# Performance work log

Measured on AMD Instinct MI355X. Metric: run time of the kernel, lower is better.

Reference implementation:

```python
import jax, jax.numpy as jnp
import numpy as np

B, S, D = 2, 2048, 1024  # batch, seq, model_dim
E, K, H = 8, 2, 4096     # experts, top_k, expert hidden
CAP_FACTOR = 1.0


def setup_inputs() -> dict:
    key = jax.random.key(0)
    ks = jax.random.split(key, 6)
    scale_in = 1.0 / np.sqrt(D)
    scale_h = 1.0 / np.sqrt(H)
    return {
        "x": jax.random.normal(ks[0], (B, S, D), jnp.float32),
        "wg": jax.random.normal(ks[1], (D, E), jnp.float32) * scale_in,
        "w1": jax.random.normal(ks[2], (E, D, H), jnp.float32) * scale_in,
        "b1": jnp.zeros((E, H), jnp.float32),
        "w2": jax.random.normal(ks[3], (E, H, D), jnp.float32) * scale_h,
        "b2": jnp.zeros((E, D), jnp.float32),
    }


def _moe_forward(x, wg, w1, b1, w2, b2):
    Bb, Ss, Dd = x.shape
    T = Bb * Ss
    cap = int(K * CAP_FACTOR * ((T + E - 1) // E))  # Tutel capacity rule
    xt = x.reshape(T, Dd)

    # ---- gating ----
    logits = xt @ wg                      # [T, E]
    scores = jax.nn.softmax(logits, axis=-1)
    gates_k, idx_k = jax.lax.top_k(scores, K)  # [T, K]
    # normalize_gate=True: renormalize top-k gates
    gates_k = gates_k / jnp.sum(gates_k, axis=-1, keepdims=True)

    # ---- GShard-style location assignment (slot-major cumsum) ----
    masks = jax.nn.one_hot(idx_k, E, dtype=jnp.int32)           # [T, K, E]
    m = jnp.transpose(masks, (1, 0, 2)).reshape(K * T, E)       # slot-major
    locs_full = jnp.cumsum(m, axis=0) - 1                       # [K*T, E]
    loc = jnp.sum(locs_full * m, axis=-1)                       # [K*T]
    loc = loc.reshape(K, T).T                                   # [T, K]
    valid = (loc < cap).astype(xt.dtype)                        # capacity drop
    loc_c = jnp.clip(loc, 0, cap - 1)

    # ---- dispatch: scatter tokens into [E, cap, D] ----
    contrib = (xt[:, None, :] * valid[:, :, None]).reshape(T * K, Dd)
    disp = jnp.zeros((E, cap, Dd), xt.dtype)
    disp = disp.at[idx_k.reshape(-1), loc_c.reshape(-1)].add(contrib)

    # ---- grouped expert FFN ----
    h = jax.nn.relu(jnp.einsum("ecd,edh->ech", disp, w1) + b1[:, None, :])
    out = jnp.einsum("ech,ehd->ecd", h, w2) + b2[:, None, :]

    # ---- combine (postscore): gather + gate-weighted sum ----
    gathered = out[idx_k, loc_c]                                # [T, K, D]
    y = jnp.einsum("tk,tkd->td", gates_k * valid, gathered)
    return y.reshape(Bb, Ss, Dd)


def reference(x, wg, w1, b1, w2, b2):
    return _moe_forward(x, wg, w1, b1, w2, b2)
```

## Files before the change

kernel.cpp:

```cpp
#include <hip/hip_runtime.h>
#include <stdint.h>

#define NTOK 4096
#define DIM  1024
#define NEXP 8
#define HID  4096
#define CAP  1024

typedef __bf16 bf16x8 __attribute__((ext_vector_type(8)));
typedef float  f32x4  __attribute__((ext_vector_type(4)));

__device__ __forceinline__ unsigned short f2bf(float f) {
  unsigned int u = __float_as_uint(f);
  return (unsigned short)((u + 0x7fffu + ((u >> 16) & 1u)) >> 16);
}

__device__ __forceinline__ float bf2f(unsigned int bits16) {
  return __uint_as_float(bits16 << 16);
}

__device__ __forceinline__ void load_lds16(const void* g, void* l) {
  __builtin_amdgcn_global_load_lds(
      (__attribute__((address_space(1))) void*)g,
      (__attribute__((address_space(3))) void*)l,
      16, 0, 0);
}

__global__ void gating_kernel(const float* __restrict__ x, const float* __restrict__ wg,
                              int* __restrict__ tok_e, float* __restrict__ tok_g) {
  const int t = blockIdx.x;
  const int l = threadIdx.x;
  float acc[NEXP];
#pragma unroll
  for (int e = 0; e < NEXP; ++e) acc[e] = 0.f;

  const float4* x4  = (const float4*)(x + (size_t)t * DIM);
  const float4* wg4 = (const float4*)wg;
#pragma unroll
  for (int i = 0; i < 4; ++i) {
    int dq = i * 64 + l;
    float4 xv = x4[dq];
    float xs[4] = {xv.x, xv.y, xv.z, xv.w};
#pragma unroll
    for (int c = 0; c < 4; ++c) {
      int d = dq * 4 + c;
      float4 wa = wg4[d * 2], wb = wg4[d * 2 + 1];
      acc[0] += xs[c] * wa.x; acc[1] += xs[c] * wa.y;
      acc[2] += xs[c] * wa.z; acc[3] += xs[c] * wa.w;
      acc[4] += xs[c] * wb.x; acc[5] += xs[c] * wb.y;
      acc[6] += xs[c] * wb.z; acc[7] += xs[c] * wb.w;
    }
  }
#pragma unroll
  for (int off = 32; off; off >>= 1)
#pragma unroll
    for (int e = 0; e < NEXP; ++e) acc[e] += __shfl_xor(acc[e], off);

  if (l == 0) {
    float m = acc[0];
#pragma unroll
    for (int e = 1; e < NEXP; ++e) m = fmaxf(m, acc[e]);
    float p[NEXP];
#pragma unroll
    for (int e = 0; e < NEXP; ++e) p[e] = __expf(acc[e] - m);
    int e0 = 0; float b0 = p[0];
#pragma unroll
    for (int e = 1; e < NEXP; ++e) if (p[e] > b0) { b0 = p[e]; e0 = e; }
    int e1 = -1; float b1v = -1.f;
#pragma unroll
    for (int e = 0; e < NEXP; ++e) if (e != e0 && p[e] > b1v) { b1v = p[e]; e1 = e; }
    float inv = 1.f / (b0 + b1v);
    tok_e[2 * t] = e0; tok_e[2 * t + 1] = e1;
    tok_g[2 * t] = b0 * inv; tok_g[2 * t + 1] = b1v * inv;
  }
}

__global__ void scan_kernel(const int* __restrict__ tok_e, int* __restrict__ tok_loc,
                            int* __restrict__ slot_map) {
  const int l = threadIdx.x;
  const unsigned long long below = (1ull << l) - 1ull;
  int base[NEXP];
#pragma unroll
  for (int e = 0; e < NEXP; ++e) base[e] = 0;

  int nxt = tok_e[((0 * 64 + l) & (NTOK - 1)) * 2 + ((0 * 64 + l) >> 12)];
  for (int it = 0; it < 128; ++it) {
    int e = nxt;
    if (it + 1 < 128) {
      int g2 = (it + 1) * 64 + l;
      nxt = tok_e[(g2 & (NTOK - 1)) * 2 + (g2 >> 12)];
    }
    int loc = 0;
#pragma unroll
    for (int ex = 0; ex < NEXP; ++ex) {
      unsigned long long msk = __ballot(e == ex);
      int off = __popcll(msk & below);
      if (e == ex) loc = base[ex] + off;
      base[ex] += __popcll(msk);
    }
    int g = it * 64 + l;
    int k = g >> 12, t = g & (NTOK - 1);
    bool valid = loc < CAP;
    tok_loc[t * 2 + k] = valid ? loc : -1;
    if (valid) slot_map[e * CAP + loc] = t;
  }
#pragma unroll
  for (int ex = 0; ex < NEXP; ++ex) {
    int c = base[ex] < CAP ? base[ex] : CAP;
    for (int i = c + l; i < CAP; i += 64) slot_map[ex * CAP + i] = -1;
  }
}

__global__ void dispatch_kernel(const float* __restrict__ x, const int* __restrict__ slot_map,
                                unsigned short* __restrict__ disp) {
  const int s = blockIdx.x;
  const int tid = threadIdx.x;
  int t = slot_map[s];
  uint2 o;
  if (t >= 0) {
    float4 v = ((const float4*)(x + (size_t)t * DIM))[tid];
    o.x = (unsigned)f2bf(v.x) | ((unsigned)f2bf(v.y) << 16);
    o.y = (unsigned)f2bf(v.z) | ((unsigned)f2bf(v.w) << 16);
  } else {
    o.x = 0u; o.y = 0u;
  }
  ((uint2*)(disp + (size_t)s * DIM))[tid] = o;
}

__global__ void transpose_cvt(const float* __restrict__ in, unsigned short* __restrict__ out,
                              int R, int C) {
  __shared__ float tile[64][65];
  const int e = blockIdx.z;
  const float* inp = in + (size_t)e * R * C;
  unsigned short* outp = out + (size_t)e * R * C;
  const int c0 = blockIdx.x * 64, r0 = blockIdx.y * 64;
  const int t = threadIdx.x;
#pragma unroll
  for (int i = 0; i < 4; ++i) {
    int idx = i * 256 + t;
    int r = idx >> 4, c4 = (idx & 15) * 4;
    float4 v = *(const float4*)(inp + (size_t)(r0 + r) * C + c0 + c4);
    tile[r][c4 + 0] = v.x; tile[r][c4 + 1] = v.y;
    tile[r][c4 + 2] = v.z; tile[r][c4 + 3] = v.w;
  }
  __syncthreads();
#pragma unroll
  for (int i = 0; i < 2; ++i) {
    int idx = i * 256 + t;
    int c = idx >> 3, r8 = (idx & 7) * 8;
    unsigned short s[8];
#pragma unroll
    for (int j = 0; j < 8; ++j) s[j] = f2bf(tile[r8 + j][c]);
    uint4 o;
    o.x = (unsigned)s[0] | ((unsigned)s[1] << 16);
    o.y = (unsigned)s[2] | ((unsigned)s[3] << 16);
    o.z = (unsigned)s[4] | ((unsigned)s[5] << 16);
    o.w = (unsigned)s[6] | ((unsigned)s[7] << 16);
    *(uint4*)(outp + (size_t)(c0 + c) * R + r0 + r8) = o;
  }
}

template <bool RELU, int MB, int NB>
__global__ __launch_bounds__(256)
void gemm_kernel(const unsigned short* __restrict__ A, const unsigned short* __restrict__ B,
                 const float* __restrict__ bias, unsigned short* __restrict__ C,
                 int N, int K) {
  constexpr int M = 1024;
  const int bid = blockIdx.x;
  const int e = bid / (MB * NB);
  const int r = bid - e * (MB * NB);
  const int patch = r / (MB * 4);
  const int q = r - patch * (MB * 4);
  const int mtile = q >> 2;
  const int ntile = patch * 4 + (q & 3);

  A += (size_t)e * M * K;
  B += (size_t)e * N * K;
  bias += (size_t)e * N;
  C += (size_t)e * M * N;
  const int m0 = mtile * 128;
  const int n0 = ntile * 128;
  const int tid = threadIdx.x;
  const int wave = tid >> 6, lane = tid & 63;
  const int wm = wave >> 1, wn = wave & 1;

  __shared__ __align__(16) unsigned short As[2][128 * 64];
  __shared__ __align__(16) unsigned short Bs[2][128 * 64];

  const int srow = lane >> 3;
  const int scol = ((lane & 7) ^ (srow & 7)) * 8;
  const unsigned short* gA = A + (size_t)(m0 + wave * 8 + srow) * K + scol;
  const unsigned short* gB = B + (size_t)(n0 + wave * 8 + srow) * K + scol;
  const int lbase = (wave * 8) * 64;

  f32x4 acc[4][4] = {};

  const int quad = lane >> 4;
  const int lxor = lane & 7;
  const int arowb = (wm * 64 + (lane & 15)) * 64;
  const int browb = (wn * 64 + (lane & 15)) * 64;

#pragma unroll
  for (int i = 0; i < 4; ++i) {
    load_lds16(gA + (size_t)i * 32 * K, &As[0][lbase + i * 32 * 64]);
    load_lds16(gB + (size_t)i * 32 * K, &Bs[0][lbase + i * 32 * 64]);
  }
  gA += 64; gB += 64;

  const int nIter = K >> 6;
  for (int it = 0; it < nIter; ++it) {
    const int cur = it & 1;
    __syncthreads();
    if (it + 1 < nIter) {
#pragma unroll
      for (int i = 0; i < 4; ++i) {
        load_lds16(gA + (size_t)i * 32 * K, &As[cur ^ 1][lbase + i * 32 * 64]);
        load_lds16(gB + (size_t)i * 32 * K, &Bs[cur ^ 1][lbase + i * 32 * 64]);
      }
      gA += 64; gB += 64;
    }
#pragma unroll
    for (int kk = 0; kk < 64; kk += 32) {
      const int coff = ((quad + (kk >> 3)) ^ lxor) * 8;
      bf16x8 af[4], bfr[4];
#pragma unroll
      for (int i = 0; i < 4; ++i)
        af[i] = *reinterpret_cast<const bf16x8*>(&As[cur][arowb + i * 16 * 64 + coff]);
#pragma unroll
      for (int j = 0; j < 4; ++j)
        bfr[j] = *reinterpret_cast<const bf16x8*>(&Bs[cur][browb + j * 16 * 64 + coff]);
#pragma unroll
      for (int i = 0; i < 4; ++i)
#pragma unroll
        for (int j = 0; j < 4; ++j)
          acc[i][j] = __builtin_amdgcn_mfma_f32_16x16x32_bf16(af[i], bfr[j], acc[i][j], 0, 0, 0);
    }
  }

  __syncthreads();
  unsigned short* scr = (wave < 2 ? &As[0][0] : &Bs[0][0]) + (wave & 1) * 4608;
  const int lc = lane & 15;
#pragma unroll
  for (int j = 0; j < 4; ++j) {
    float bj = bias[n0 + wn * 64 + j * 16 + lc];
#pragma unroll
    for (int i = 0; i < 4; ++i)
#pragma unroll
      for (int rr = 0; rr < 4; ++rr) {
        float v = acc[i][j][rr] + bj;
        if (RELU) v = fmaxf(v, 0.f);
        scr[(i * 16 + quad * 4 + rr) * 72 + j * 16 + lc] = f2bf(v);
      }
  }
  __asm__ volatile("s_waitcnt lgkmcnt(0)" ::: "memory");
  const int erow = lane >> 3;
  const int ecol = (lane & 7) * 8;
  unsigned short* Cbase = C + (size_t)(m0 + wm * 64) * N + n0 + wn * 64;
#pragma unroll
  for (int p = 0; p < 8; ++p) {
    uint4 v = *(const uint4*)&scr[(p * 8 + erow) * 72 + ecol];
    *(uint4*)&Cbase[(size_t)(p * 8 + erow) * N + ecol] = v;
  }
}

__global__ void combine_kernel(const unsigned short* __restrict__ outb,
                               const int* __restrict__ tok_e, const int* __restrict__ tok_loc,
                               const float* __restrict__ tok_g, float* __restrict__ y) {
  const int t = blockIdx.x;
  const int tid = threadIdx.x;
  int e0 = tok_e[2 * t], e1 = tok_e[2 * t + 1];
  int l0 = tok_loc[2 * t], l1 = tok_loc[2 * t + 1];
  float g0 = tok_g[2 * t], g1 = tok_g[2 * t + 1];
  float ax = 0.f, ay = 0.f, az = 0.f, aw = 0.f;
  if (l0 >= 0) {
    uint2 u = ((const uint2*)(outb + ((size_t)e0 * CAP + l0) * DIM))[tid];
    ax += g0 * bf2f(u.x & 0xffffu); ay += g0 * __uint_as_float(u.x & 0xffff0000u);
    az += g0 * bf2f(u.y & 0xffffu); aw += g0 * __uint_as_float(u.y & 0xffff0000u);
  }
  if (l1 >= 0) {
    uint2 u = ((const uint2*)(outb + ((size_t)e1 * CAP + l1) * DIM))[tid];
    ax += g1 * bf2f(u.x & 0xffffu); ay += g1 * __uint_as_float(u.x & 0xffff0000u);
    az += g1 * bf2f(u.y & 0xffffu); aw += g1 * __uint_as_float(u.y & 0xffff0000u);
  }
  float4 o; o.x = ax; o.y = ay; o.z = az; o.w = aw;
  ((float4*)(y + (size_t)t * DIM))[tid] = o;
}

extern "C" void kernel_launch(void* const* d_in, const int* in_sizes, int n_in,
                              void* d_out, int out_size, void* d_ws, size_t ws_size,
                              hipStream_t stream) {
  const float* x  = (const float*)d_in[0];
  const float* wg = (const float*)d_in[1];
  const float* w1 = (const float*)d_in[2];
  const float* b1 = (const float*)d_in[3];
  const float* w2 = (const float*)d_in[4];
  const float* b2 = (const float*)d_in[5];
  float* y = (float*)d_out;

  char* ws = (char*)d_ws;
  int*   tok_e    = (int*)(ws);
  int*   tok_loc  = (int*)(ws + 32768);
  float* tok_g    = (float*)(ws + 65536);
  int*   slot_map = (int*)(ws + 98304);
  unsigned short* disp = (unsigned short*)(ws + 131072);
  unsigned short* wbuf = (unsigned short*)(ws + 131072 + (16ull << 20));
  unsigned short* h    = (unsigned short*)(ws + 131072 + (80ull << 20));
  unsigned short* outb = (unsigned short*)(ws + 131072 + (144ull << 20));

  gating_kernel<<<NTOK, 64, 0, stream>>>(x, wg, tok_e, tok_g);
  scan_kernel<<<1, 64, 0, stream>>>(tok_e, tok_loc, slot_map);
  dispatch_kernel<<<NEXP * CAP, 256, 0, stream>>>(x, slot_map, disp);
  transpose_cvt<<<dim3(HID / 64, DIM / 64, NEXP), 256, 0, stream>>>(w1, wbuf, DIM, HID);
  gemm_kernel<true, 8, 32><<<NEXP * 8 * 32, 256, 0, stream>>>(disp, wbuf, b1, h, HID, DIM);
  transpose_cvt<<<dim3(DIM / 64, HID / 64, NEXP), 256, 0, stream>>>(w2, wbuf, HID, DIM);
  gemm_kernel<false, 8, 8><<<NEXP * 8 * 8, 256, 0, stream>>>(h, wbuf, b2, outb, DIM, HID);
  combine_kernel<<<NTOK, 256, 0, stream>>>(outb, tok_e, tok_loc, tok_g, y);
}
```

Before: 541.4 us.

## Rewrite expert GEMMs as 8-wave large-tile kernels with 4-phase pipelined LDS staging

Replaces the 128x128 4-wave expert GEMM with a 512-thread kernel using 256x256 tiles for the first GEMM and 128x256 for the second. The K loop is split into four quadrant phases, each issuing the next global-to-LDS loads while running MFMAs, with explicit vmcnt waits, barriers and setprio. The goal is more data reuse per tile and overlap of memory traffic with tensor-core work. The cost is large dynamic shared memory (up to 128KB), hence low occupancy and fewer blocks for the second GEMM (256 blocks), plus fragile hand-written wait counts.

```diff
diff --git a/kernel.cpp b/kernel.cpp
--- a/kernel.cpp
+++ b/kernel.cpp
@@ -160,106 +160,160 @@
   }
 }
 
-template <bool RELU, int MB, int NB>
-__global__ __launch_bounds__(256)
-void gemm_kernel(const unsigned short* __restrict__ A, const unsigned short* __restrict__ B,
-                 const float* __restrict__ bias, unsigned short* __restrict__ C,
-                 int N, int K) {
+template <int BM, int BN, bool RELU>
+__global__ __launch_bounds__(512)
+void gemm8(const unsigned short* __restrict__ A, const unsigned short* __restrict__ B,
+           const float* __restrict__ bias, unsigned short* __restrict__ C,
+           int N, int K) {
   constexpr int M = 1024;
+  constexpr int FR = BM / 64;
+  constexpr int FC = BN / 128;
+  constexpr int ASLOT = (BM / 2) * 64;
+  constexpr int BSLOT = (BN / 2) * 64;
+  constexpr int LA = BM / 128;
+  constexpr int LB = BN / 128;
+  static_assert(LA + LB == 4 || LA + LB == 3, "vmcnt literal");
+
+  extern __shared__ __align__(16) unsigned short smem[];
+  unsigned short* As = smem;
+  unsigned short* Bs = smem + 4 * ASLOT;
+
+  const int mt = M / BM;
+  const int ntn = N / BN;
   const int bid = blockIdx.x;
-  const int e = bid / (MB * NB);
-  const int r = bid - e * (MB * NB);
-  const int patch = r / (MB * 4);
-  const int q = r - patch * (MB * 4);
-  const int mtile = q >> 2;
-  const int ntile = patch * 4 + (q & 3);
+  const int e = bid / (mt * ntn);
+  const int rb = bid - e * mt * ntn;
+  const int mtile = rb / ntn;
+  const int ntile = rb - mtile * ntn;
 
   A += (size_t)e * M * K;
   B += (size_t)e * N * K;
   bias += (size_t)e * N;
   C += (size_t)e * M * N;
-  const int m0 = mtile * 128;
-  const int n0 = ntile * 128;
+  const int m0 = mtile * BM;
+  const int n0 = ntile * BN;
+
   const int tid = threadIdx.x;
-  const int wave = tid >> 6, lane = tid & 63;
-  const int wm = wave >> 1, wn = wave & 1;
-
-  __shared__ __align__(16) unsigned short As[2][128 * 64];
-  __shared__ __align__(16) unsigned short Bs[2][128 * 64];
+  const int w = tid >> 6, lane = tid & 63;
+  const int wm = w >> 2, wn = w & 3;
 
   const int srow = lane >> 3;
-  const int scol = ((lane & 7) ^ (srow & 7)) * 8;
-  const unsigned short* gA = A + (size_t)(m0 + wave * 8 + srow) * K + scol;
-  const unsigned short* gB = B + (size_t)(n0 + wave * 8 + srow) * K + scol;
-  const int lbase = (wave * 8) * 64;
-
-  f32x4 acc[4][4] = {};
-
-  const int quad = lane >> 4;
-  const int lxor = lane & 7;
-  const int arowb = (wm * 64 + (lane & 15)) * 64;
-  const int browb = (wn * 64 + (lane & 15)) * 64;
-
-#pragma unroll
-  for (int i = 0; i < 4; ++i) {
-    load_lds16(gA + (size_t)i * 32 * K, &As[0][lbase + i * 32 * 64]);
-    load_lds16(gB + (size_t)i * 32 * K, &Bs[0][lbase + i * 32 * 64]);
-  }
-  gA += 64; gB += 64;
-
-  const int nIter = K >> 6;
-  for (int it = 0; it < nIter; ++it) {
-    const int cur = it & 1;
+  const int scol = ((lane & 7) ^ srow) * 8;
+  const unsigned short* gA = A + (size_t)(m0 + w * 8 + srow) * K + scol;
+  const unsigned short* gB = B + (size_t)(n0 + w * 8 + srow) * K + scol;
+  const int lbase = w * 512;
+
+  const int arow0 = wm * (BM / 4) + (lane & 15);
+  const int brow0 = wn * (BN / 8) + (lane & 15);
+  const int c0 = (((lane >> 4) + 0) ^ (lane & 7)) * 8;
+  const int c1 = (((lane >> 4) + 4) ^ (lane & 7)) * 8;
+
+  f32x4 acc[2][2][FR][FC] = {};
+  const int nt = K >> 6;
+
+#define STAGE_A(T, MH) do {                                                        \
+    const unsigned short* g_ = gA + (size_t)((MH) * (BM / 2)) * K + (size_t)(T) * 64; \
+    unsigned short* l_ = &As[(2 * ((T) & 1) + (MH)) * ASLOT + lbase];              \
+    _Pragma("unroll")                                                              \
+    for (int q_ = 0; q_ < LA; ++q_)                                                \
+      load_lds16(g_ + (size_t)q_ * 64 * K, l_ + q_ * 4096);                        \
+  } while (0)
+
+#define STAGE_B(T, NH) do {                                                        \
+    const unsigned short* g_ = gB + (size_t)((NH) * (BN / 2)) * K + (size_t)(T) * 64; \
+    unsigned short* l_ = &Bs[(2 * ((T) & 1) + (NH)) * BSLOT + lbase];              \
+    _Pragma("unroll")                                                              \
+    for (int q_ = 0; q_ < LB; ++q_)                                                \
+      load_lds16(g_ + (size_t)q_ * 64 * K, l_ + q_ * 4096);                        \
+  } while (0)
+
+#define WAIT_VMN() do {                                                            \
+    if constexpr (LA + LB == 4) asm volatile("s_waitcnt vmcnt(4)" ::: "memory");   \
+    else                        asm volatile("s_waitcnt vmcnt(3)" ::: "memory");   \
+  } while (0)
+
+#define PHASE(MH, NH, ISVM, ...) do {                                              \
+    bf16x8 af[FR][2], bfv[FC][2];                                                  \
+    const unsigned short* ab_ = &As[(2 * cur + (MH)) * ASLOT + arow0 * 64];        \
+    const unsigned short* bb_ = &Bs[(2 * cur + (NH)) * BSLOT + brow0 * 64];        \
+    _Pragma("unroll")                                                              \
+    for (int f_ = 0; f_ < FR; ++f_) {                                              \
+      af[f_][0] = *(const bf16x8*)(ab_ + f_ * 1024 + c0);                          \
+      af[f_][1] = *(const bf16x8*)(ab_ + f_ * 1024 + c1);                          \
+    }                                                                              \
+    _Pragma("unroll")                                                              \
+    for (int f_ = 0; f_ < FC; ++f_) {                                              \
+      bfv[f_][0] = *(const bf16x8*)(bb_ + f_ * 1024 + c0);                         \
+      bfv[f_][1] = *(const bf16x8*)(bb_ + f_ * 1024 + c1);                         \
+    }                                                                              \
+    __VA_ARGS__                                                                    \
+    __builtin_amdgcn_s_barrier();                                                  \
+    asm volatile("s_waitcnt lgkmcnt(0)" ::: "memory");                             \
+    __builtin_amdgcn_sched_barrier(0);                                             \
+    __builtin_amdgcn_s_setprio(1);                                                 \
+    _Pragma("unroll")                                                              \
+    for (int f_ = 0; f_ < FR; ++f_)                                                \
+      _Pragma("unroll")                                                            \
+      for (int g_ = 0; g_ < FC; ++g_) {                                            \
+        acc[MH][NH][f_][g_] = __builtin_amdgcn_mfma_f32_16x16x32_bf16(             \
+            af[f_][0], bfv[g_][0], acc[MH][NH][f_][g_], 0, 0, 0);                  \
+        acc[MH][NH][f_][g_] = __builtin_amdgcn_mfma_f32_16x16x32_bf16(             \
+            af[f_][1], bfv[g_][1], acc[MH][NH][f_][g_], 0, 0, 0);                  \
+      }                                                                            \
+    __builtin_amdgcn_s_setprio(0);                                                 \
+    if (ISVM) WAIT_VMN();                                                          \
+    asm volatile("" ::: "memory");                                                 \
+    __builtin_amdgcn_s_barrier();                                                  \
+  } while (0)
+
+  STAGE_A(0, 0); STAGE_A(0, 1); STAGE_B(0, 0); STAGE_B(0, 1);
+  STAGE_B(1, 0); STAGE_A(1, 0);
+  WAIT_VMN();
+  __builtin_amdgcn_s_barrier();
+
+  for (int t = 0; t < nt; ++t) {
+    const int cur = t & 1;
+    const bool s1 = (t + 1) < nt, s2 = (t + 2) < nt;
+    PHASE(0, 0, false, if (s1) STAGE_A(t + 1, 1); );
+    PHASE(1, 0, false, if (s1) STAGE_B(t + 1, 1); );
+    PHASE(0, 1, false, if (s2) STAGE_B(t + 2, 0); );
+    PHASE(1, 1, true,  if (s2) STAGE_A(t + 2, 0); );
+  }
+
+#undef PHASE
+#undef WAIT_VMN
+#undef STAGE_B
+#undef STAGE_A
+
+  const int lc = lane & 15, quad = lane >> 4;
+  constexpr int SW = BN + 8;
+  unsigned short* scr = smem;
+#pragma unroll
+  for (int Mh = 0; Mh < 2; ++Mh) {
     __syncthreads();
-    if (it + 1 < nIter) {
-#pragma unroll
-      for (int i = 0; i < 4; ++i) {
-        load_lds16(gA + (size_t)i * 32 * K, &As[cur ^ 1][lbase + i * 32 * 64]);
-        load_lds16(gB + (size_t)i * 32 * K, &Bs[cur ^ 1][lbase + i * 32 * 64]);
-      }
-      gA += 64; gB += 64;
+#pragma unroll
+    for (int Nh = 0; Nh < 2; ++Nh)
+#pragma unroll
+      for (int f = 0; f < FR; ++f)
+#pragma unroll
+        for (int g = 0; g < FC; ++g) {
+          float bv = bias[n0 + Nh * (BN / 2) + wn * (BN / 8) + g * 16 + lc];
+#pragma unroll
+          for (int r2 = 0; r2 < 4; ++r2) {
+            float v = acc[Mh][Nh][f][g][r2] + bv;
+            if (RELU) v = fmaxf(v, 0.f);
+            scr[(wm * (BM / 4) + f * 16 + quad * 4 + r2) * SW +
+                Nh * (BN / 2) + wn * (BN / 8) + g * 16 + lc] = f2bf(v);
+          }
+        }
+    __syncthreads();
+#pragma unroll
+    for (int it = 0; it < (BM / 2) * (BN / 8) / 512; ++it) {
+      const int u = it * 512 + tid;
+      const int row = u / (BN / 8), seg = u % (BN / 8);
+      uint4 v = *(const uint4*)&scr[row * SW + seg * 8];
+      *(uint4*)&C[(size_t)(m0 + Mh * (BM / 2) + row) * N + n0 + seg * 8] = v;
     }
-#pragma unroll
-    for (int kk = 0; kk < 64; kk += 32) {
-      const int coff = ((quad + (kk >> 3)) ^ lxor) * 8;
-      bf16x8 af[4], bfr[4];
-#pragma unroll
-      for (int i = 0; i < 4; ++i)
-        af[i] = *reinterpret_cast<const bf16x8*>(&As[cur][arowb + i * 16 * 64 + coff]);
-#pragma unroll
-      for (int j = 0; j < 4; ++j)
-        bfr[j] = *reinterpret_cast<const bf16x8*>(&Bs[cur][browb + j * 16 * 64 + coff]);
-#pragma unroll
-      for (int i = 0; i < 4; ++i)
-#pragma unroll
-        for (int j = 0; j < 4; ++j)
-          acc[i][j] = __builtin_amdgcn_mfma_f32_16x16x32_bf16(af[i], bfr[j], acc[i][j], 0, 0, 0);
-    }
-  }
-
-  __syncthreads();
-  unsigned short* scr = (wave < 2 ? &As[0][0] : &Bs[0][0]) + (wave & 1) * 4608;
-  const int lc = lane & 15;
-#pragma unroll
-  for (int j = 0; j < 4; ++j) {
-    float bj = bias[n0 + wn * 64 + j * 16 + lc];
-#pragma unroll
-    for (int i = 0; i < 4; ++i)
-#pragma unroll
-      for (int rr = 0; rr < 4; ++rr) {
-        float v = acc[i][j][rr] + bj;
-        if (RELU) v = fmaxf(v, 0.f);
-        scr[(i * 16 + quad * 4 + rr) * 72 + j * 16 + lc] = f2bf(v);
-      }
-  }
-  __asm__ volatile("s_waitcnt lgkmcnt(0)" ::: "memory");
-  const int erow = lane >> 3;
-  const int ecol = (lane & 7) * 8;
-  unsigned short* Cbase = C + (size_t)(m0 + wm * 64) * N + n0 + wn * 64;
-#pragma unroll
-  for (int p = 0; p < 8; ++p) {
-    uint4 v = *(const uint4*)&scr[(p * 8 + erow) * 72 + ecol];
-    *(uint4*)&Cbase[(size_t)(p * 8 + erow) * N + ecol] = v;
   }
 }
 
@@ -307,12 +361,23 @@
   unsigned short* h    = (unsigned short*)(ws + 131072 + (80ull << 20));
   unsigned short* outb = (unsigned short*)(ws + 131072 + (144ull << 20));
 
+  static int att = 0;
+  if (!att) {
+    (void)hipFuncSetAttribute(reinterpret_cast<const void*>(&gemm8<256, 256, true>),
+                              hipFuncAttributeMaxDynamicSharedMemorySize, 131072);
+    (void)hipFuncSetAttribute(reinterpret_cast<const void*>(&gemm8<128, 256, false>),
+                              hipFuncAttributeMaxDynamicSharedMemorySize, 98304);
+    att = 1;
+  }
+
   gating_kernel<<<NTOK, 64, 0, stream>>>(x, wg, tok_e, tok_g);
   scan_kernel<<<1, 64, 0, stream>>>(tok_e, tok_loc, slot_map);
   dispatch_kernel<<<NEXP * CAP, 256, 0, stream>>>(x, slot_map, disp);
   transpose_cvt<<<dim3(HID / 64, DIM / 64, NEXP), 256, 0, stream>>>(w1, wbuf, DIM, HID);
-  gemm_kernel<true, 8, 32><<<NEXP * 8 * 32, 256, 0, stream>>>(disp, wbuf, b1, h, HID, DIM);
+  gemm8<256, 256, true><<<NEXP * (1024 / 256) * (HID / 256), 512, 131072, stream>>>(
+      disp, wbuf, b1, h, HID, DIM);
   transpose_cvt<<<dim3(DIM / 64, HID / 64, NEXP), 256, 0, stream>>>(w2, wbuf, HID, DIM);
-  gemm_kernel<false, 8, 8><<<NEXP * 8 * 8, 256, 0, stream>>>(h, wbuf, b2, outb, DIM, HID);
+  gemm8<128, 256, false><<<NEXP * (1024 / 128) * (DIM / 256), 512, 98304, stream>>>(
+      h, wbuf, b2, outb, DIM, HID);
   combine_kernel<<<NTOK, 256, 0, stream>>>(outb, tok_e, tok_loc, tok_g, y);
 }
```

Measured after the change: 523.1 us. 3.4% less time.

## Shrink GEMM K-tile to 32 for higher occupancy, remap blocks across XCDs

Applied to the files above, without the earlier changes.

The GEMM now uses a K-step of 32 instead of 64, which halves LDS per block (16 KB) and adds a launch-bounds hint targeting 4 blocks per CU. Block IDs are remapped so consecutive tiles of the same expert land on the same XCD for L2 reuse. The epilogue is split into two 32-row halves to fit the smaller scratch, and the weight transpose now processes 128-row tiles per block. The cost is twice as many barriers per K, plus possible register spills under the tighter launch bound.

```diff
diff --git a/kernel.cpp b/kernel.cpp
--- a/kernel.cpp
+++ b/kernel.cpp
@@ -129,14 +129,14 @@
 
 __global__ void transpose_cvt(const float* __restrict__ in, unsigned short* __restrict__ out,
                               int R, int C) {
-  __shared__ float tile[64][65];
+  __shared__ float tile[128][65];
   const int e = blockIdx.z;
   const float* inp = in + (size_t)e * R * C;
   unsigned short* outp = out + (size_t)e * R * C;
-  const int c0 = blockIdx.x * 64, r0 = blockIdx.y * 64;
+  const int c0 = blockIdx.x * 64, r0 = blockIdx.y * 128;
   const int t = threadIdx.x;
 #pragma unroll
-  for (int i = 0; i < 4; ++i) {
+  for (int i = 0; i < 8; ++i) {
     int idx = i * 256 + t;
     int r = idx >> 4, c4 = (idx & 15) * 4;
     float4 v = *(const float4*)(inp + (size_t)(r0 + r) * C + c0 + c4);
@@ -145,9 +145,9 @@
   }
   __syncthreads();
 #pragma unroll
-  for (int i = 0; i < 2; ++i) {
+  for (int i = 0; i < 4; ++i) {
     int idx = i * 256 + t;
-    int c = idx >> 3, r8 = (idx & 7) * 8;
+    int c = idx >> 4, r8 = (idx & 15) * 8;
     unsigned short s[8];
 #pragma unroll
     for (int j = 0; j < 8; ++j) s[j] = f2bf(tile[r8 + j][c]);
@@ -160,106 +160,107 @@
   }
 }
 
-template <bool RELU, int MB, int NB>
-__global__ __launch_bounds__(256)
+template <bool RELU>
+__global__ __launch_bounds__(256, 4)
 void gemm_kernel(const unsigned short* __restrict__ A, const unsigned short* __restrict__ B,
                  const float* __restrict__ bias, unsigned short* __restrict__ C,
                  int N, int K) {
-  constexpr int M = 1024;
-  const int bid = blockIdx.x;
-  const int e = bid / (MB * NB);
-  const int r = bid - e * (MB * NB);
-  const int patch = r / (MB * 4);
-  const int q = r - patch * (MB * 4);
-  const int mtile = q >> 2;
-  const int ntile = patch * 4 + (q & 3);
-
-  A += (size_t)e * M * K;
+  __shared__ __align__(16) unsigned short As[2][128 * 32];
+  __shared__ __align__(16) unsigned short Bs[2][128 * 32];
+
+  int bid = blockIdx.x;
+  const int cpx = (int)gridDim.x >> 3;
+  bid = (bid & 7) * cpx + (bid >> 3);
+  const int ntn = N >> 7;
+  const int per_e = 8 * ntn;
+  const int e = bid / per_e;
+  const int rb = bid - e * per_e;
+  const int mtile = rb / ntn;
+  const int ntile = rb - mtile * ntn;
+
+  A += (size_t)e * 1024 * K;
   B += (size_t)e * N * K;
   bias += (size_t)e * N;
-  C += (size_t)e * M * N;
+  C += (size_t)e * 1024 * N;
   const int m0 = mtile * 128;
   const int n0 = ntile * 128;
+
   const int tid = threadIdx.x;
   const int wave = tid >> 6, lane = tid & 63;
   const int wm = wave >> 1, wn = wave & 1;
-
-  __shared__ __align__(16) unsigned short As[2][128 * 64];
-  __shared__ __align__(16) unsigned short Bs[2][128 * 64];
-
-  const int srow = lane >> 3;
-  const int scol = ((lane & 7) ^ (srow & 7)) * 8;
-  const unsigned short* gA = A + (size_t)(m0 + wave * 8 + srow) * K + scol;
-  const unsigned short* gB = B + (size_t)(n0 + wave * 8 + srow) * K + scol;
-  const int lbase = (wave * 8) * 64;
+  const int quad = lane >> 4;
+
+  const int srow = lane >> 2;
+  const int scol = ((lane & 3) ^ (srow & 3)) * 8;
+  const unsigned short* gA = A + (size_t)(m0 + wave * 16 + srow) * K + scol;
+  const unsigned short* gB = B + (size_t)(n0 + wave * 16 + srow) * K + scol;
 
   f32x4 acc[4][4] = {};
 
-  const int quad = lane >> 4;
-  const int lxor = lane & 7;
-  const int arowb = (wm * 64 + (lane & 15)) * 64;
-  const int browb = (wn * 64 + (lane & 15)) * 64;
-
-#pragma unroll
-  for (int i = 0; i < 4; ++i) {
-    load_lds16(gA + (size_t)i * 32 * K, &As[0][lbase + i * 32 * 64]);
-    load_lds16(gB + (size_t)i * 32 * K, &Bs[0][lbase + i * 32 * 64]);
-  }
-  gA += 64; gB += 64;
-
-  const int nIter = K >> 6;
-  for (int it = 0; it < nIter; ++it) {
-    const int cur = it & 1;
+  const int coff = (quad ^ (lane & 3)) * 8;
+  const int arowb = (wm * 64 + (lane & 15)) * 32;
+  const int browb = (wn * 64 + (lane & 15)) * 32;
+
+#pragma unroll
+  for (int i = 0; i < 2; ++i) {
+    load_lds16(gA + (size_t)i * 64 * K, &As[0][(i * 64 + wave * 16) * 32]);
+    load_lds16(gB + (size_t)i * 64 * K, &Bs[0][(i * 64 + wave * 16) * 32]);
+  }
+  gA += 32; gB += 32;
+
+  const int nIter = K >> 5;
+  for (int t = 0; t < nIter; ++t) {
+    const int cur = t & 1;
     __syncthreads();
-    if (it + 1 < nIter) {
-#pragma unroll
-      for (int i = 0; i < 4; ++i) {
-        load_lds16(gA + (size_t)i * 32 * K, &As[cur ^ 1][lbase + i * 32 * 64]);
-        load_lds16(gB + (size_t)i * 32 * K, &Bs[cur ^ 1][lbase + i * 32 * 64]);
+    if (t + 1 < nIter) {
+#pragma unroll
+      for (int i = 0; i < 2; ++i) {
+        load_lds16(gA + (size_t)i * 64 * K, &As[cur ^ 1][(i * 64 + wave * 16) * 32]);
+        load_lds16(gB + (size_t)i * 64 * K, &Bs[cur ^ 1][(i * 64 + wave * 16) * 32]);
       }
-      gA += 64; gB += 64;
-    }
-#pragma unroll
-    for (int kk = 0; kk < 64; kk += 32) {
-      const int coff = ((quad + (kk >> 3)) ^ lxor) * 8;
-      bf16x8 af[4], bfr[4];
-#pragma unroll
-      for (int i = 0; i < 4; ++i)
-        af[i] = *reinterpret_cast<const bf16x8*>(&As[cur][arowb + i * 16 * 64 + coff]);
+      gA += 32; gB += 32;
+    }
+    bf16x8 af[4], bfr[4];
+#pragma unroll
+    for (int i = 0; i < 4; ++i)
+      af[i] = *reinterpret_cast<const bf16x8*>(&As[cur][arowb + i * 512 + coff]);
+#pragma unroll
+    for (int j = 0; j < 4; ++j)
+      bfr[j] = *reinterpret_cast<const bf16x8*>(&Bs[cur][browb + j * 512 + coff]);
+#pragma unroll
+    for (int i = 0; i < 4; ++i)
 #pragma unroll
       for (int j = 0; j < 4; ++j)
-        bfr[j] = *reinterpret_cast<const bf16x8*>(&Bs[cur][browb + j * 16 * 64 + coff]);
-#pragma unroll
-      for (int i = 0; i < 4; ++i)
-#pragma unroll
-        for (int j = 0; j < 4; ++j)
-          acc[i][j] = __builtin_amdgcn_mfma_f32_16x16x32_bf16(af[i], bfr[j], acc[i][j], 0, 0, 0);
-    }
+        acc[i][j] = __builtin_amdgcn_mfma_f32_16x16x32_bf16(af[i], bfr[j], acc[i][j], 0, 0, 0);
   }
 
   __syncthreads();
-  unsigned short* scr = (wave < 2 ? &As[0][0] : &Bs[0][0]) + (wave & 1) * 4608;
+  unsigned short* scr = (wave < 2 ? &As[0][0] : &Bs[0][0]) + (wave & 1) * 2304;
   const int lc = lane & 15;
-#pragma unroll
-  for (int j = 0; j < 4; ++j) {
-    float bj = bias[n0 + wn * 64 + j * 16 + lc];
-#pragma unroll
-    for (int i = 0; i < 4; ++i)
-#pragma unroll
-      for (int rr = 0; rr < 4; ++rr) {
-        float v = acc[i][j][rr] + bj;
-        if (RELU) v = fmaxf(v, 0.f);
-        scr[(i * 16 + quad * 4 + rr) * 72 + j * 16 + lc] = f2bf(v);
-      }
-  }
-  __asm__ volatile("s_waitcnt lgkmcnt(0)" ::: "memory");
   const int erow = lane >> 3;
   const int ecol = (lane & 7) * 8;
-  unsigned short* Cbase = C + (size_t)(m0 + wm * 64) * N + n0 + wn * 64;
-#pragma unroll
-  for (int p = 0; p < 8; ++p) {
-    uint4 v = *(const uint4*)&scr[(p * 8 + erow) * 72 + ecol];
-    *(uint4*)&Cbase[(size_t)(p * 8 + erow) * N + ecol] = v;
+#pragma unroll
+  for (int p = 0; p < 2; ++p) {
+#pragma unroll
+    for (int j = 0; j < 4; ++j) {
+      float bj = bias[n0 + wn * 64 + j * 16 + lc];
+#pragma unroll
+      for (int ii = 0; ii < 2; ++ii) {
+#pragma unroll
+        for (int rr = 0; rr < 4; ++rr) {
+          float v = acc[p * 2 + ii][j][rr] + bj;
+          if (RELU) v = fmaxf(v, 0.f);
+          scr[(ii * 16 + quad * 4 + rr) * 72 + j * 16 + lc] = f2bf(v);
+        }
+      }
+    }
+    __asm__ volatile("s_waitcnt lgkmcnt(0)" ::: "memory");
+    unsigned short* Cbase = C + (size_t)(m0 + wm * 64 + p * 32) * N + n0 + wn * 64;
+#pragma unroll
+    for (int pp = 0; pp < 4; ++pp) {
+      uint4 v = *(const uint4*)&scr[(pp * 8 + erow) * 72 + ecol];
+      *(uint4*)&Cbase[(size_t)(pp * 8 + erow) * N + ecol] = v;
+    }
   }
 }
 
@@ -310,9 +311,9 @@
   gating_kernel<<<NTOK, 64, 0, stream>>>(x, wg, tok_e, tok_g);
   scan_kernel<<<1, 64, 0, stream>>>(tok_e, tok_loc, slot_map);
   dispatch_kernel<<<NEXP * CAP, 256, 0, stream>>>(x, slot_map, disp);
-  transpose_cvt<<<dim3(HID / 64, DIM / 64, NEXP), 256, 0, stream>>>(w1, wbuf, DIM, HID);
-  gemm_kernel<true, 8, 32><<<NEXP * 8 * 32, 256, 0, stream>>>(disp, wbuf, b1, h, HID, DIM);
-  transpose_cvt<<<dim3(DIM / 64, HID / 64, NEXP), 256, 0, stream>>>(w2, wbuf, HID, DIM);
-  gemm_kernel<false, 8, 8><<<NEXP * 8 * 8, 256, 0, stream>>>(h, wbuf, b2, outb, DIM, HID);
+  transpose_cvt<<<dim3(HID / 64, DIM / 128, NEXP), 256, 0, stream>>>(w1, wbuf, DIM, HID);
+  gemm_kernel<true><<<NEXP * 8 * (HID / 128), 256, 0, stream>>>(disp, wbuf, b1, h, HID, DIM);
+  transpose_cvt<<<dim3(DIM / 64, HID / 128, NEXP), 256, 0, stream>>>(w2, wbuf, HID, DIM);
+  gemm_kernel<false><<<NEXP * 8 * (DIM / 128), 256, 0, stream>>>(h, wbuf, b2, outb, DIM, HID);
   combine_kernel<<<NTOK, 256, 0, stream>>>(outb, tok_e, tok_loc, tok_g, y);
 }
```

After: 559.2 us. 1.03x slower.
